# Kernel optimization log

Hardware: AMD Instinct MI355X
Metric: run time of the kernel (lower is better)

The kernel has to match this reference:

```python
import jax, jax.numpy as jnp
import numpy as np

T = 0.07
TOPK = 5

def _l2norm(x, axis=-1, eps=1e-12):
    n = jnp.sqrt(jnp.sum(x * x, axis=axis, keepdims=True))
    return x / jnp.maximum(n, eps)

def setup_inputs() -> dict:
    key = jax.random.key(0)
    k1, k2, k3, k4, k5 = jax.random.split(key, 5)
    b, nc, dim, dim_mlp, K = 256, 5, 128, 2048, 65536
    q = jax.random.normal(k1, (b, nc, dim), jnp.float32)
    k = jax.random.normal(k2, (b, dim), jnp.float32)
    q_backbone = jax.random.normal(k3, (b, nc, dim_mlp), jnp.float32)
    # queues are column-normalized buffers, as in __init__
    queue = _l2norm(jax.random.normal(k4, (dim, K), jnp.float32), axis=0)
    queue_backbone = _l2norm(jax.random.normal(k5, (dim_mlp, K), jnp.float32), axis=0)
    return {"q": q, "k": k, "q_backbone": q_backbone,
            "queue": queue, "queue_backbone": queue_backbone}

def reference(q, k, q_backbone, queue, queue_backbone):
    b, nc, dim = q.shape
    dim_mlp = q_backbone.shape[-1]
    qn = _l2norm(q)                 # [b, nc, dim]
    kn = _l2norm(k)                 # [b, dim]
    qb = _l2norm(q_backbone)        # [b, nc, dim_mlp]

    # positive logits: each crop vs its key
    l_pos = jnp.einsum('bnd,bd->bn', qn, kn).reshape(-1, 1)      # [b*nc, 1]
    # negative logits vs queue
    l_neg = jnp.einsum('nc,ck->nk', qn.reshape(-1, dim), queue)  # [b*nc, K]
    logits = jnp.concatenate([l_pos, l_neg], axis=1) / T
    labels = jnp.zeros((logits.shape[0],), dtype=jnp.int32)

    # backbone-space similarities to pick top-k neighbors
    l_neg_backbone = jnp.einsum('nc,ck->nk', qb.reshape(-1, dim_mlp), queue_backbone)

    # pull_topk: softmax CE pulling toward top-k backbone neighbors.
    # scatter-mask + masked mean == gather log-softmax at top-k indices (indices distinct)
    _, knn_idx = jax.lax.top_k(l_neg_backbone, TOPK)             # [b*nc, TOPK]
    log_prob = jax.nn.log_softmax(l_neg / T, axis=1)             # [b*nc, K]
    pos_logp = jnp.take_along_axis(log_prob, knn_idx, axis=1)    # [b*nc, TOPK]
    loss = -jnp.mean(jnp.mean(pos_logp, axis=1))
    return logits, labels, loss
```

## Files before the change

kernel.cpp:

```cpp
#include <hip/hip_runtime.h>
#include <hip/hip_bf16.h>
#include <hip/hip_fp8.h>

#define M_     1280
#define DIM    128
#define DMLP   2048
#define KQ     65536
#define NCOLS  65537ull
#define NTOPK  5
#define NCHUNK 1024
#define NBLK1  512
#define NTK    32
#define INV_T  14.285714285714286f

typedef __attribute__((ext_vector_type(8))) short bf16x8;
typedef __attribute__((ext_vector_type(4))) float f32x4;
typedef __attribute__((ext_vector_type(2))) long longx2;

static __device__ __forceinline__ unsigned short f2bf(float x){
  union { __hip_bfloat16 h; unsigned short u; } cv;
  cv.h = __float2bfloat16(x);
  return cv.u;
}

static __device__ __forceinline__ unsigned char f2f8(float x){
  __hip_fp8_e4m3 h(x);
  return (unsigned char)h.__x;
}

#define GLDS16(gp, lp) __builtin_amdgcn_global_load_lds( \
    (const __attribute__((address_space(1))) void*)(gp), \
    (__attribute__((address_space(3))) void*)(lp), 16, 0, 0)

#define BAR()   asm volatile("s_barrier" ::: "memory")
#define VMW(n)  asm volatile("s_waitcnt vmcnt(" #n ")" ::: "memory")

__global__ __launch_bounds__(256) void transpose_bf16(
    const float* __restrict__ in, unsigned short* __restrict__ out, int R, int C){
  __shared__ float tile[64][65];
  const int c0 = blockIdx.x * 64, r0 = blockIdx.y * 64;
  const int t = threadIdx.x;
  #pragma unroll
  for (int i = 0; i < 4; ++i){
    int lin = t + i * 256;
    int rr = lin >> 4;
    int cc = (lin & 15) * 4;
    const float4 v = *(const float4*)(in + (size_t)(r0 + rr) * C + c0 + cc);
    tile[rr][cc + 0] = v.x; tile[rr][cc + 1] = v.y;
    tile[rr][cc + 2] = v.z; tile[rr][cc + 3] = v.w;
  }
  __syncthreads();
  #pragma unroll
  for (int i = 0; i < 4; ++i){
    int lin = t + i * 256;
    int oc  = lin >> 4;
    int orr = (lin & 15) * 4;
    ushort4 u;
    u.x = f2bf(tile[orr + 0][oc]); u.y = f2bf(tile[orr + 1][oc]);
    u.z = f2bf(tile[orr + 2][oc]); u.w = f2bf(tile[orr + 3][oc]);
    *(ushort4*)(out + (size_t)(c0 + oc) * R + r0 + orr) = u;
  }
}

__global__ __launch_bounds__(256) void transpose_fp8(
    const float* __restrict__ in, unsigned char* __restrict__ out, int R, int C){
  __shared__ float tile[64][65];
  const int c0 = blockIdx.x * 64, r0 = blockIdx.y * 64;
  const int t = threadIdx.x;
  #pragma unroll
  for (int i = 0; i < 4; ++i){
    int lin = t + i * 256;
    int rr = lin >> 4;
    int cc = (lin & 15) * 4;
    const float4 v = *(const float4*)(in + (size_t)(r0 + rr) * C + c0 + cc);
    tile[rr][cc + 0] = v.x; tile[rr][cc + 1] = v.y;
    tile[rr][cc + 2] = v.z; tile[rr][cc + 3] = v.w;
  }
  __syncthreads();
  #pragma unroll
  for (int i = 0; i < 4; ++i){
    int lin = t + i * 256;
    int oc  = lin >> 4;
    int orr = (lin & 15) * 4;
    const int quad  = (orr >> 3) & 3;
    const int slice = orr >> 5;
    const int sub   = orr & 7;
    uchar4 u;
    u.x = f2f8(tile[orr + 0][oc]); u.y = f2f8(tile[orr + 1][oc]);
    u.z = f2f8(tile[orr + 2][oc]); u.w = f2f8(tile[orr + 3][oc]);
    *(uchar4*)(out + (size_t)(c0 + oc) * R + r0 + quad * 16 + slice * 8 + sub) = u;
  }
}

__global__ __launch_bounds__(128) void normq_kernel(
    const float* __restrict__ q, const float* __restrict__ k,
    unsigned short* __restrict__ qn, float* __restrict__ outp){
  const int i = blockIdx.x;
  const int t = threadIdx.x;
  const float qv = q[(size_t)i * DIM + t];
  const float kv = k[(size_t)(i / 5) * DIM + t];
  float a = qv * qv, b = kv * kv, d = qv * kv;
  #pragma unroll
  for (int s = 32; s >= 1; s >>= 1){
    a += __shfl_down(a, s, 64);
    b += __shfl_down(b, s, 64);
    d += __shfl_down(d, s, 64);
  }
  __shared__ float red[6];
  if ((t & 63) == 0){ red[(t >> 6) * 3 + 0] = a; red[(t >> 6) * 3 + 1] = b; red[(t >> 6) * 3 + 2] = d; }
  __syncthreads();
  const float qq = red[0] + red[3], kk = red[1] + red[4], qk = red[2] + red[5];
  const float qnorm = fmaxf(sqrtf(qq), 1e-12f);
  qn[(size_t)i * DIM + t] = f2bf(qv / qnorm);
  if (t == 0){
    const float knorm = fmaxf(sqrtf(kk), 1e-12f);
    outp[(size_t)i * NCOLS] = (qk / (qnorm * knorm)) * INV_T;
  }
}

__global__ __launch_bounds__(256) void normqb_kernel(
    const float* __restrict__ qb, unsigned char* __restrict__ out){
  const int i = blockIdx.x, t = threadIdx.x;
  const float* p = qb + (size_t)i * DMLP;
  float x[8]; float ss = 0.f;
  #pragma unroll
  for (int j = 0; j < 8; ++j){ x[j] = p[t + j * 256]; ss += x[j] * x[j]; }
  #pragma unroll
  for (int s = 32; s >= 1; s >>= 1) ss += __shfl_down(ss, s, 64);
  __shared__ float r4[4];
  if ((t & 63) == 0) r4[t >> 6] = ss;
  __syncthreads();
  const float tot = r4[0] + r4[1] + r4[2] + r4[3];
  const float inv = 1.0f / fmaxf(sqrtf(tot), 1e-12f);
  unsigned char* o = out + (size_t)i * DMLP;
  #pragma unroll
  for (int j = 0; j < 8; ++j){
    const int kx = t + j * 256;
    const int kk = kx & 63;
    const int pos = (kx & ~63) + ((kk >> 3) & 3) * 16 + (kk >> 5) * 8 + (kk & 7);
    o[pos] = f2f8(x[j] * inv);
  }
}

static __device__ __forceinline__ void tk_insert(float* v, int* ix, float nv, int ni){
  if (nv > v[4]){
    v[4] = nv; ix[4] = ni;
    #pragma unroll
    for (int j = 4; j > 0; --j){
      if (v[j] > v[j - 1]){
        float tv = v[j]; v[j] = v[j - 1]; v[j - 1] = tv;
        int   ti = ix[j]; ix[j] = ix[j - 1]; ix[j - 1] = ti;
      }
    }
  }
}

__global__ __launch_bounds__(256, 2) void gemm1_mfma(
    const unsigned short* __restrict__ A, const unsigned short* __restrict__ BT,
    float* __restrict__ outp, float* __restrict__ pm, float* __restrict__ ps){
  __shared__ __attribute__((aligned(16))) unsigned char smem[65536];
  unsigned short* At = (unsigned short*)smem;
  unsigned short* Bt = At + 16384;

  const int t    = threadIdx.x;
  const int lane = t & 63;
  const int wv   = t >> 6;
  const int lid  = lane & 15;
  const int quad = lane >> 4;
  const int m0 = blockIdx.x * 128;
  const int n0 = blockIdx.y * 128;

  f32x4 acc[2][8];
  #pragma unroll
  for (int mt = 0; mt < 2; ++mt)
    #pragma unroll
    for (int nt = 0; nt < 8; ++nt)
      acc[mt][nt] = f32x4{0.f, 0.f, 0.f, 0.f};

  const int arow = t >> 2;
  const int ace  = (t & 3) * 8;

  #pragma unroll
  for (int kt = 0; kt < 4; ++kt)
    #pragma unroll
    for (int it = 0; it < 2; ++it){
      const int row = arow + it * 64;
      GLDS16(A + (size_t)(m0 + row) * DIM + kt * 32 + ace,
             At + kt * 4096 + (t + it * 256) * 8);
    }
  #pragma unroll
  for (int kt = 0; kt < 4; ++kt)
    #pragma unroll
    for (int it = 0; it < 2; ++it){
      const int row = arow + it * 64;
      GLDS16(BT + (size_t)(n0 + row) * DIM + kt * 32 + ace,
             Bt + kt * 4096 + (t + it * 256) * 8);
    }
  VMW(0);
  BAR();

  for (int kt = 0; kt < 4; ++kt){
    bf16x8 af[2], bfr[8];
    #pragma unroll
    for (int mt = 0; mt < 2; ++mt)
      af[mt] = *(const bf16x8*)(At + kt * 4096 + (wv * 32 + mt * 16 + lid) * 32 + quad * 8);
    #pragma unroll
    for (int nt = 0; nt < 8; ++nt)
      bfr[nt] = *(const bf16x8*)(Bt + kt * 4096 + (nt * 16 + lid) * 32 + quad * 8);
    #pragma unroll
    for (int mt = 0; mt < 2; ++mt)
      #pragma unroll
      for (int nt = 0; nt < 8; ++nt)
        acc[mt][nt] = __builtin_amdgcn_mfma_f32_16x16x32_bf16(af[mt], bfr[nt], acc[mt][nt], 0, 0, 0);
  }

  float mx[2][4], sm[2][4];
  #pragma unroll
  for (int mt = 0; mt < 2; ++mt)
    #pragma unroll
    for (int r = 0; r < 4; ++r) mx[mt][r] = -3.0e38f;
  #pragma unroll
  for (int mt = 0; mt < 2; ++mt)
    #pragma unroll
    for (int nt = 0; nt < 8; ++nt)
      #pragma unroll
      for (int r = 0; r < 4; ++r){
        const int mg = m0 + wv * 32 + mt * 16 + quad * 4 + r;
        const int ng = n0 + nt * 16 + lid;
        const float x = acc[mt][nt][r] * INV_T;
        outp[(size_t)mg * NCOLS + 1 + ng] = x;
        mx[mt][r] = fmaxf(mx[mt][r], x);
      }
  #pragma unroll
  for (int mt = 0; mt < 2; ++mt)
    #pragma unroll
    for (int r = 0; r < 4; ++r){
      #pragma unroll
      for (int s = 8; s >= 1; s >>= 1)
        mx[mt][r] = fmaxf(mx[mt][r], __shfl_xor(mx[mt][r], s, 64));
      sm[mt][r] = 0.f;
    }
  #pragma unroll
  for (int mt = 0; mt < 2; ++mt)
    #pragma unroll
    for (int nt = 0; nt < 8; ++nt)
      #pragma unroll
      for (int r = 0; r < 4; ++r)
        sm[mt][r] += __expf(acc[mt][nt][r] * INV_T - mx[mt][r]);
  #pragma unroll
  for (int mt = 0; mt < 2; ++mt)
    #pragma unroll
    for (int r = 0; r < 4; ++r){
      #pragma unroll
      for (int s = 8; s >= 1; s >>= 1)
        sm[mt][r] += __shfl_xor(sm[mt][r], s, 64);
      if (lid == 0){
        const int mg = m0 + wv * 32 + mt * 16 + quad * 4 + r;
        pm[(size_t)mg * NBLK1 + blockIdx.y] = mx[mt][r];
        ps[(size_t)mg * NBLK1 + blockIdx.y] = sm[mt][r];
      }
    }
}


#define RDA8(SRC) do { _Pragma("unroll") for (int mf = 0; mf < 4; ++mf) \
    av[mf] = *(const longx2*)((SRC) + (wm * 64 + mf * 16 + lid) * 64 + qsw); } while(0)

#define RDB8(SRC) do { _Pragma("unroll") for (int nf = 0; nf < 4; ++nf) \
    bv[nf] = *(const longx2*)((SRC) + (wn * 64 + nf * 16 + lid) * 64 + qsw); } while(0)

#define MM_NF(nj_) do { \
    _Pragma("unroll") for (int mf = 0; mf < 4; ++mf){ \
      acc[mf][nj_] = __builtin_amdgcn_mfma_f32_16x16x32_fp8_fp8(av[mf].x, bv[nj_].x, acc[mf][nj_], 0, 0, 0); \
      acc[mf][nj_] = __builtin_amdgcn_mfma_f32_16x16x32_fp8_fp8(av[mf].y, bv[nj_].y, acc[mf][nj_], 0, 0, 0); } } while(0)

__global__ __launch_bounds__(512, 4) void gemm2_topk(
    const unsigned char* __restrict__ A, const unsigned char* __restrict__ BT,
    float* __restrict__ cval, int* __restrict__ cidx){
  __shared__ __attribute__((aligned(16))) unsigned char smem[73728];

  const int t    = threadIdx.x;
  const int lane = t & 63;
  const int wv   = t >> 6;
  const int wm   = wv >> 1;
  const int wn   = wv & 1;
  const int lid  = lane & 15;
  const int quad = lane >> 4;
  const int qsw  = (quad ^ (lid & 3)) * 16;

  const int h  = blockIdx.x;
  const int wg = (h & 7) * 320 + (h >> 3);
  const int bm = wg % 5;
  const int bn = wg / 5;
  const int m0 = bm * 256;
  const int n0 = bn * 128;

  const int srow = t >> 2;
  const size_t roff = (size_t)srow * DMLP + (size_t)(((t & 3) ^ (srow & 3)) * 16);
  const unsigned char* aB = A  + (size_t)m0 * DMLP;
  const unsigned char* bB = BT + (size_t)n0 * DMLP;

  f32x4 acc[4][4];
  #pragma unroll
  for (int a = 0; a < 4; ++a)
    #pragma unroll
    for (int b = 0; b < 4; ++b)
      acc[a][b] = f32x4{0.f, 0.f, 0.f, 0.f};

  longx2 av[4];
  longx2 bv[4];

  #define STAGE2(kt_, bi_) do { \
    unsigned char* _a = smem + (bi_) * 24576; \
    const int _kc = (kt_) * 64; \
    GLDS16(aB + roff + _kc, _a + (size_t)t * 16); \
    GLDS16(aB + roff + 128 * DMLP + _kc, _a + (size_t)(512 + t) * 16); \
    GLDS16(bB + roff + _kc, _a + 16384 + (size_t)t * 16); } while(0)

  STAGE2(0, 0);
  STAGE2(1, 1);
  VMW(3);
  BAR();

  for (int kt = 0; kt < NTK; ++kt){
    const int bi = kt % 3;
    unsigned char* curA = smem + bi * 24576;
    unsigned char* curB = curA + 16384;

    RDA8(curA);
    RDB8(curB);

    if (kt + 2 < NTK) STAGE2(kt + 2, (kt + 2) % 3);

    __builtin_amdgcn_s_setprio(1);
    MM_NF(0); MM_NF(1); MM_NF(2); MM_NF(3);
    __builtin_amdgcn_s_setprio(0);

    if (kt + 1 < NTK){
      if (kt + 2 < NTK){ VMW(3); } else { VMW(0); }
      BAR();
    }
  }

  float* scratch = (float*)smem;
  BAR();
  #pragma unroll
  for (int p = 0; p < 2; ++p){
    if ((wm >> 1) == p){
      #pragma unroll
      for (int mf = 0; mf < 4; ++mf)
        #pragma unroll
        for (int nf = 0; nf < 4; ++nf)
          #pragma unroll
          for (int r = 0; r < 4; ++r){
            const int lr = (wm & 1) * 64 + mf * 16 + quad * 4 + r;
            scratch[lr * 133 + wn * 64 + nf * 16 + lid] = acc[mf][nf][r];
          }
    }
    __syncthreads();
    {
      const int lr    = t >> 2;
      const int seg   = t & 3;
      const int chunk = seg >> 1;
      float v[5]; int ix[5];
      #pragma unroll
      for (int j = 0; j < 5; ++j){ v[j] = -3.0e38f; ix[j] = 0; }
      const int cb0 = chunk * 64 + (seg & 1) * 32;
      for (int j = 0; j < 32; ++j)
        tk_insert(v, ix, scratch[lr * 133 + cb0 + j], n0 + cb0 + j);
      #pragma unroll
      for (int j = 0; j < 5; ++j){
        const float pv = __shfl_xor(v[j], 1, 64);
        const int   pi = __shfl_xor(ix[j], 1, 64);
        if ((t & 1) == 0) tk_insert(v, ix, pv, pi);
      }
      if ((t & 1) == 0){
        const int rowg = m0 + p * 128 + lr;
        const size_t cb = ((size_t)rowg * NCHUNK + bn * 2 + chunk) * NTOPK;
        #pragma unroll
        for (int j = 0; j < 5; ++j){ cval[cb + j] = v[j]; cidx[cb + j] = ix[j]; }
      }
    }
    __syncthreads();
  }
}

__global__ __launch_bounds__(256) void topk_merge(
    const float* __restrict__ cval, const int* __restrict__ cidx, int* __restrict__ knn){
  const int row = blockIdx.x, t = threadIdx.x;
  float v[5]; int ix[5];
  #pragma unroll
  for (int j = 0; j < 5; ++j){ v[j] = -3.0e38f; ix[j] = 0; }
  const size_t base = (size_t)row * (NCHUNK * NTOPK);
  #pragma unroll
  for (int j = 0; j < 20; ++j){
    const int c = t * 20 + j;
    tk_insert(v, ix, cval[base + c], cidx[base + c]);
  }
  __shared__ float lv[256 * 5];
  __shared__ int   li[256 * 5];
  #pragma unroll
  for (int j = 0; j < 5; ++j){ lv[t * 5 + j] = v[j]; li[t * 5 + j] = ix[j]; }
  __syncthreads();
  if (t < 64){
    float v2[5]; int ix2[5];
    #pragma unroll
    for (int j = 0; j < 5; ++j){ v2[j] = -3.0e38f; ix2[j] = 0; }
    for (int L = 0; L < 4; ++L)
      #pragma unroll
      for (int j = 0; j < 5; ++j)
        tk_insert(v2, ix2, lv[(t * 4 + L) * 5 + j], li[(t * 4 + L) * 5 + j]);
    #pragma unroll
    for (int s = 32; s >= 1; s >>= 1){
      float pv[5]; int pi[5];
      #pragma unroll
      for (int j = 0; j < 5; ++j){ pv[j] = __shfl_down(v2[j], s, 64); pi[j] = __shfl_down(ix2[j], s, 64); }
      #pragma unroll
      for (int j = 0; j < 5; ++j) tk_insert(v2, ix2, pv[j], pi[j]);
    }
    if (t == 0){
      #pragma unroll
      for (int j = 0; j < 5; ++j) knn[(size_t)row * NTOPK + j] = ix2[j];
    }
  }
}

__global__ __launch_bounds__(256) void lse_merge(
    const float* __restrict__ pm, const float* __restrict__ ps,
    float* __restrict__ lse){
  const int row = blockIdx.x, t = threadIdx.x;
  const float* pmr = pm + (size_t)row * NBLK1;
  const float* psr = ps + (size_t)row * NBLK1;
  float m = -1.0e30f, s = 0.f;
  #pragma unroll
  for (int c = 0; c < 2; ++c){
    const float om = pmr[t + c * 256], os = psr[t + c * 256];
    const float nm = fmaxf(m, om);
    s = s * __expf(m - nm) + os * __expf(om - nm);
    m = nm;
  }
  #pragma unroll
  for (int sh = 32; sh >= 1; sh >>= 1){
    const float om = __shfl_down(m, sh, 64), os = __shfl_down(s, sh, 64);
    const float nm = fmaxf(m, om);
    s = s * __expf(m - nm) + os * __expf(om - nm);
    m = nm;
  }
  __shared__ float sm2[4], ss2[4];
  if ((t & 63) == 0){ sm2[t >> 6] = m; ss2[t >> 6] = s; }
  __syncthreads();
  if (t == 0){
    float M = sm2[0], S = ss2[0];
    #pragma unroll
    for (int w = 1; w < 4; ++w){
      const float nm = fmaxf(M, sm2[w]);
      S = S * __expf(M - nm) + ss2[w] * __expf(sm2[w] - nm);
      M = nm;
    }
    lse[row] = M + __logf(S);
  }
}

__global__ __launch_bounds__(256) void loss_kernel(
    const float* __restrict__ logits, const float* __restrict__ lse,
    const int* __restrict__ knn, float* __restrict__ loss){
  const int i = blockIdx.x * 256 + threadIdx.x;
  float c = 0.f;
  if (i < M_){
    const float l = lse[i];
    #pragma unroll
    for (int j = 0; j < 5; ++j){
      const int id = knn[(size_t)i * NTOPK + j];
      c += l - logits[(size_t)i * NCOLS + 1 + id];
    }
    c *= (1.0f / 6400.0f);
  }
  #pragma unroll
  for (int s = 32; s >= 1; s >>= 1) c += __shfl_down(c, s, 64);
  if ((threadIdx.x & 63) == 0) atomicAdd(loss, c);
}

extern "C" void kernel_launch(void* const* d_in, const int* in_sizes, int n_in,
                              void* d_out, int out_size, void* d_ws, size_t ws_size,
                              hipStream_t stream){
  const float* q   = (const float*)d_in[0];
  const float* k   = (const float*)d_in[1];
  const float* qbI = (const float*)d_in[2];
  const float* que = (const float*)d_in[3];
  const float* qbb = (const float*)d_in[4];
  float* out = (float*)d_out;

  unsigned char* w = (unsigned char*)d_ws;
  unsigned short* qn    = (unsigned short*)w; w += (size_t)M_ * DIM  * 2;
  unsigned char*  qbn8  = (unsigned char*)w;  w += (size_t)M_ * DMLP;
  unsigned short* queT  = (unsigned short*)w; w += (size_t)KQ * DIM  * 2;
  unsigned char*  qbbT8 = (unsigned char*)w;  w += (size_t)KQ * DMLP;
  float* cval = (float*)w;                    w += (size_t)M_ * NCHUNK * NTOPK * 4;
  int*   cidx = (int*)w;                      w += (size_t)M_ * NCHUNK * NTOPK * 4;
  int*   knn  = (int*)w;                      w += (size_t)M_ * NTOPK * 4;
  float* lseb = (float*)w;                    w += (size_t)M_ * 4;
  float* pm   = (float*)w;                    w += (size_t)M_ * NBLK1 * 4;
  float* ps   = (float*)w;                    w += (size_t)M_ * NBLK1 * 4;

  hipMemsetAsync(out + (size_t)M_ * NCOLS, 0, (M_ + 1) * sizeof(float), stream);

  transpose_bf16<<<dim3(KQ / 64, DIM  / 64), 256, 0, stream>>>(que, queT, DIM, KQ);
  transpose_fp8 <<<dim3(KQ / 64, DMLP / 64), 256, 0, stream>>>(qbb, qbbT8, DMLP, KQ);
  normq_kernel <<<M_, 128, 0, stream>>>(q, k, qn, out);
  normqb_kernel<<<M_, 256, 0, stream>>>(qbI, qbn8);
  gemm1_mfma<<<dim3(10, NBLK1), 256, 0, stream>>>(qn, queT, out, pm, ps);
  gemm2_topk<<<dim3(2560), 512, 0, stream>>>(qbn8, qbbT8, cval, cidx);
  topk_merge<<<M_, 256, 0, stream>>>(cval, cidx, knn);
  lse_merge<<<M_, 256, 0, stream>>>(pm, ps, lseb);
  loss_kernel<<<(M_ + 255) / 256, 256, 0, stream>>>(out, lseb, knn,
                                                    out + (size_t)M_ * NCOLS + M_);
}
```

Measured before the change: 1.273 ms.

## Remap gemm1 blocks across XCDs and halve top-k chunk candidates

```diff
diff --git a/kernel.cpp b/kernel.cpp
--- a/kernel.cpp
+++ b/kernel.cpp
@@ -8,7 +8,7 @@
 #define KQ     65536
 #define NCOLS  65537ull
 #define NTOPK  5
-#define NCHUNK 1024
+#define NCHUNK 512
 #define NBLK1  512
 #define NTK    32
 #define INV_T  14.285714285714286f
@@ -167,8 +167,12 @@
   const int wv   = t >> 6;
   const int lid  = lane & 15;
   const int quad = lane >> 4;
-  const int m0 = blockIdx.x * 128;
-  const int n0 = blockIdx.y * 128;
+  const int h  = blockIdx.x;
+  const int wg = (h & 7) * 640 + (h >> 3);
+  const int bm = wg % 10;
+  const int bn = wg / 10;
+  const int m0 = bm * 128;
+  const int n0 = bn * 128;
 
   f32x4 acc[2][8];
   #pragma unroll
@@ -256,8 +260,8 @@
         sm[mt][r] += __shfl_xor(sm[mt][r], s, 64);
       if (lid == 0){
         const int mg = m0 + wv * 32 + mt * 16 + quad * 4 + r;
-        pm[(size_t)mg * NBLK1 + blockIdx.y] = mx[mt][r];
-        ps[(size_t)mg * NBLK1 + blockIdx.y] = sm[mt][r];
+        pm[(size_t)mg * NBLK1 + bn] = mx[mt][r];
+        ps[(size_t)mg * NBLK1 + bn] = sm[mt][r];
       }
     }
 }
@@ -359,24 +363,25 @@
     }
     __syncthreads();
     {
-      const int lr    = t >> 2;
-      const int seg   = t & 3;
-      const int chunk = seg >> 1;
+      const int lr  = t >> 2;
+      const int seg = t & 3;
       float v[5]; int ix[5];
       #pragma unroll
       for (int j = 0; j < 5; ++j){ v[j] = -3.0e38f; ix[j] = 0; }
-      const int cb0 = chunk * 64 + (seg & 1) * 32;
+      const int cb0 = seg * 32;
       for (int j = 0; j < 32; ++j)
         tk_insert(v, ix, scratch[lr * 133 + cb0 + j], n0 + cb0 + j);
       #pragma unroll
-      for (int j = 0; j < 5; ++j){
-        const float pv = __shfl_xor(v[j], 1, 64);
-        const int   pi = __shfl_xor(ix[j], 1, 64);
-        if ((t & 1) == 0) tk_insert(v, ix, pv, pi);
+      for (int s = 1; s <= 2; s <<= 1){
+        float pv[5]; int pi[5];
+        #pragma unroll
+        for (int j = 0; j < 5; ++j){ pv[j] = __shfl_xor(v[j], s, 64); pi[j] = __shfl_xor(ix[j], s, 64); }
+        #pragma unroll
+        for (int j = 0; j < 5; ++j) tk_insert(v, ix, pv[j], pi[j]);
       }
-      if ((t & 1) == 0){
+      if (seg == 0){
         const int rowg = m0 + p * 128 + lr;
-        const size_t cb = ((size_t)rowg * NCHUNK + bn * 2 + chunk) * NTOPK;
+        const size_t cb = ((size_t)rowg * NCHUNK + bn) * NTOPK;
         #pragma unroll
         for (int j = 0; j < 5; ++j){ cval[cb + j] = v[j]; cidx[cb + j] = ix[j]; }
       }
@@ -393,8 +398,8 @@
   for (int j = 0; j < 5; ++j){ v[j] = -3.0e38f; ix[j] = 0; }
   const size_t base = (size_t)row * (NCHUNK * NTOPK);
   #pragma unroll
-  for (int j = 0; j < 20; ++j){
-    const int c = t * 20 + j;
+  for (int j = 0; j < 10; ++j){
+    const int c = t * 10 + j;
     tk_insert(v, ix, cval[base + c], cidx[base + c]);
   }
   __shared__ float lv[256 * 5];
@@ -508,7 +513,7 @@
   transpose_fp8 <<<dim3(KQ / 64, DMLP / 64), 256, 0, stream>>>(qbb, qbbT8, DMLP, KQ);
   normq_kernel <<<M_, 128, 0, stream>>>(q, k, qn, out);
   normqb_kernel<<<M_, 256, 0, stream>>>(qbI, qbn8);
-  gemm1_mfma<<<dim3(10, NBLK1), 256, 0, stream>>>(qn, queT, out, pm, ps);
+  gemm1_mfma<<<dim3(5120), 256, 0, stream>>>(qn, queT, out, pm, ps);
   gemm2_topk<<<dim3(2560), 512, 0, stream>>>(qbn8, qbbT8, cval, cidx);
   topk_merge<<<M_, 256, 0, stream>>>(cval, cidx, knn);
   lse_merge<<<M_, 256, 0, stream>>>(pm, ps, lseb);
```

Measured after the change: 1.195 ms. 1.07x faster.
